# Optimization experiments

Hardware: AMD Instinct MI355X
Metric: run time of the kernel (lower is better)

Reference implementation:

```python
import jax, jax.numpy as jnp
import numpy as np

N_NODES = 100000
N_EDGES = 1600000
IN_CH = 128
TYPE_EMB = 32
OUT_CH = 128
N_REL = 8
N_BASES = 8
N_NTYPES = 8
FEAT = IN_CH + TYPE_EMB  # 160, RGCNConv input dim after concat


def setup_inputs() -> dict:
    key = jax.random.key(0)
    ks = jax.random.split(key, 9)
    x = jax.random.normal(ks[0], (N_NODES, IN_CH), dtype=jnp.float32)
    node_type_ids = jax.random.randint(ks[1], (N_NODES,), 0, N_NTYPES)
    edge_index = jax.random.randint(ks[2], (2, N_EDGES), 0, N_NODES)
    edge_type = jax.random.randint(ks[3], (N_EDGES,), 0, N_REL)
    emb_table = jax.random.normal(ks[4], (N_NTYPES, TYPE_EMB), dtype=jnp.float32)
    bases = jax.random.normal(ks[5], (N_BASES, FEAT, OUT_CH), dtype=jnp.float32) * (1.0 / np.sqrt(FEAT))
    comp = jax.random.normal(ks[6], (N_REL, N_BASES), dtype=jnp.float32) * (1.0 / np.sqrt(N_BASES))
    root_w = jax.random.normal(ks[7], (FEAT, OUT_CH), dtype=jnp.float32) * (1.0 / np.sqrt(FEAT))
    bias = jnp.zeros((OUT_CH,), dtype=jnp.float32)
    return {"x": x, "node_type_ids": node_type_ids, "edge_index": edge_index,
            "edge_type": edge_type, "emb_table": emb_table, "bases": bases,
            "comp": comp, "root_w": root_w, "bias": bias}


def reference(x, node_type_ids, edge_index, edge_type, emb_table, bases, comp, root_w, bias):
    N = x.shape[0]
    # node-type embedding lookup + concat
    h = jnp.concatenate([x, emb_table[node_type_ids]], axis=1)  # [N, FEAT]
    # basis decomposition: per-relation weights [R, FEAT, OUT]
    weight = jnp.einsum('rb,bio->rio', comp, bases)
    src, dst = edge_index[0], edge_index[1]
    h_src = h[src]  # [E, FEAT] -- dominant gather
    # root/self transform + bias
    out = h @ root_w + bias
    # PyG RGCNConv default aggr='mean': per-relation mean over incoming edges, summed across relations
    for r in range(weight.shape[0]):
        m = (edge_type == r).astype(h.dtype)  # [E]
        s = jax.ops.segment_sum(h_src * m[:, None], dst, num_segments=N)  # [N, FEAT]
        c = jax.ops.segment_sum(m, dst, num_segments=N)                    # [N]
        mean_r = s / jnp.maximum(c, 1.0)[:, None]
        out = out + mean_r @ weight[r]
    # dropout is identity in eval mode
    return jax.nn.relu(out)
```

## Files before the change

### kernel.cpp

```cpp
#include <hip/hip_runtime.h>

#define NN 100000
#define NE 1600000
#define INC 128
#define TE 32
#define OC 128
#define NR 8
#define NBASES 8
#define FT 160
#define KP 168
#define KW 160
#define TN 32
#define NBKT 3125
#define NCH 128
#define EPB 12500
#define CAP 896

typedef float f32x4 __attribute__((ext_vector_type(4)));
typedef float f32x2 __attribute__((ext_vector_type(2)));
typedef __bf16 bf16x8 __attribute__((ext_vector_type(8)));

__device__ __forceinline__ unsigned f2bf1(float f) {
    unsigned u = __float_as_uint(f);
    return (u + 0x7fffu + ((u >> 16) & 1u)) >> 16;
}

__device__ __forceinline__ float bflo(unsigned u) { return __uint_as_float(u << 16); }
__device__ __forceinline__ float bfhi(unsigned u) { return __uint_as_float(u & 0xFFFF0000u); }

__device__ __forceinline__ unsigned cvtpk(float a, float b) {
    unsigned r;
    asm("v_cvt_pk_bf16_f32 %0, %1, %2" : "=v"(r) : "v"(a), "v"(b));
    return r;
}

__device__ __forceinline__ int bscan_excl(int v, int* tmp) {
    int tid = threadIdx.x;
    tmp[tid] = v; __syncthreads();
#pragma unroll
    for (int d = 1; d < 256; d <<= 1) {
        int t = (tid >= d) ? tmp[tid - d] : 0;
        __syncthreads();
        tmp[tid] += t;
        __syncthreads();
    }
    return tmp[tid] - v;
}

__global__ __launch_bounds__(256) void k_prep(
    const float* __restrict__ x, const int* __restrict__ nt,
    const float* __restrict__ emb, const float* __restrict__ comp,
    const float* __restrict__ bases, const float* __restrict__ rootw,
    const int* __restrict__ ei,
    unsigned short* __restrict__ h, unsigned short* __restrict__ Wt,
    int* __restrict__ ghist) {
    __shared__ int hist[NBKT];
    int tid = threadIdx.x;
    int b = blockIdx.x;
    if (b < NCH) {
        for (int j = tid; j < NBKT; j += 256) hist[j] = 0;
        __syncthreads();
        int e0 = b * EPB;
#pragma unroll
        for (int k = 0; k < 49; k++) {
            int i = k * 256 + tid;
            if (i < EPB) atomicAdd(&hist[ei[NE + e0 + i] >> 5], 1);
        }
        __syncthreads();
        int* g = ghist + (size_t)b * NBKT;
        for (int j = tid; j < NBKT; j += 256) g[j] = hist[j];
        return;
    }
    int idx = (b - NCH) * 256 + tid;
    if (idx < 9 * 128 * KW) {
        int ridx = idx / (128 * KW);
        int rem  = idx % (128 * KW);
        int o = rem / KW;
        int k = rem % KW;
        float v;
        if (ridx < NR) {
            v = 0.f;
#pragma unroll
            for (int bb = 0; bb < NBASES; bb++)
                v += comp[ridx * NBASES + bb] * bases[(bb * FT + k) * OC + o];
        } else {
            v = rootw[k * OC + o];
        }
        Wt[idx] = (unsigned short)f2bf1(v);
    }
    if (idx < NN * 20) {
        int n = idx / 20, c = idx % 20;
        f32x4 v0, v1;
        if (c < 16) {
            const float* p = x + (size_t)n * INC + c * 8;
            v0 = *(const f32x4*)p; v1 = *(const f32x4*)(p + 4);
        } else {
            int tt = nt[n];
            const float* p = emb + tt * TE + (c - 16) * 8;
            v0 = *(const f32x4*)p; v1 = *(const f32x4*)(p + 4);
        }
        uint4 o;
        o.x = f2bf1(v0.x) | (f2bf1(v0.y) << 16);
        o.y = f2bf1(v0.z) | (f2bf1(v0.w) << 16);
        o.z = f2bf1(v1.x) | (f2bf1(v1.y) << 16);
        o.w = f2bf1(v1.z) | (f2bf1(v1.w) << 16);
        *(uint4*)(h + (size_t)n * FT + c * 8) = o;
    }
}

__global__ void k_total(const int* __restrict__ ghist, int* __restrict__ total) {
    int j = blockIdx.x * 256 + threadIdx.x;
    if (j >= NBKT) return;
    int s = 0;
#pragma unroll 8
    for (int b = 0; b < NCH; b++) s += ghist[(size_t)b * NBKT + j];
    total[j] = s;
}

__global__ void k_scanTot(const int* __restrict__ total, int* __restrict__ bstart) {
    __shared__ int tmp[256];
    int tid = threadIdx.x, s = 0, i0 = tid * 13;
#pragma unroll
    for (int i = 0; i < 13; i++) { int j = i0 + i; if (j < NBKT) s += total[j]; }
    int run = bscan_excl(s, tmp);
#pragma unroll
    for (int i = 0; i < 13; i++) { int j = i0 + i; if (j < NBKT) { bstart[j] = run; run += total[j]; } }
    if (tid == 0) bstart[NBKT] = NE;
}

__global__ void k_offsets(int* __restrict__ ghist, const int* __restrict__ bstart) {
    int j = blockIdx.x * 256 + threadIdx.x;
    if (j >= NBKT) return;
    int run = bstart[j];
#pragma unroll 4
    for (int b = 0; b < NCH; b++) {
        int v = ghist[(size_t)b * NBKT + j];
        ghist[(size_t)b * NBKT + j] = run;
        run += v;
    }
}

__global__ __launch_bounds__(256) void k_scatter(const int* __restrict__ ei, const int* __restrict__ et,
                                                 const int* __restrict__ ghist, unsigned* __restrict__ slots) {
    __shared__ int cur[NBKT];
    int tid = threadIdx.x, b = blockIdx.x;
    for (int j = tid; j < NBKT; j += 256) cur[j] = ghist[(size_t)b * NBKT + j];
    __syncthreads();
    int e0 = b * EPB;
#pragma unroll
    for (int k = 0; k < 49; k++) {
        int i = k * 256 + tid;
        if (i < EPB) {
            int e = e0 + i;
            int s = ei[e], d = ei[NE + e], r = et[e];
            int pos = atomicAdd(&cur[d >> 5], 1);
            slots[pos] = (unsigned)s | ((unsigned)r << 17) | ((unsigned)(d & 31) << 20);
        }
    }
}

__global__ __launch_bounds__(256, 6) void k_mega(
    const unsigned short* __restrict__ h, const float* __restrict__ bias,
    const unsigned short* __restrict__ Wt, const int* __restrict__ bstart,
    const unsigned* __restrict__ slots, float* __restrict__ out) {
    __shared__ unsigned short featmem[TN * KP];
    __shared__ unsigned sl[CAP];
    __shared__ unsigned pkl[256];

    const int tid = threadIdx.x;
    const int lane = tid & 63;
    const int wave = tid >> 6;
    const int j = blockIdx.x;
    const int n0 = j * TN;

    unsigned* sl_in = reinterpret_cast<unsigned*>(featmem);
    int* hist = reinterpret_cast<int*>(featmem) + CAP;
    int* tmp  = reinterpret_cast<int*>(featmem) + CAP + 256;

    int s0 = bstart[j];
    int m = bstart[j + 1] - s0; if (m > CAP) m = CAP;
    for (int i = tid; i < m; i += 256) sl_in[i] = slots[s0 + i];
    hist[tid] = 0;
    __syncthreads();
    for (int i = tid; i < m; i += 256) {
        unsigned v = sl_in[i];
        atomicAdd(&hist[((v >> 17) & 7u) * 32u + ((v >> 20) & 31u)], 1);
    }
    __syncthreads();
    int v0 = hist[tid];
    int ex = bscan_excl(v0, tmp);
    pkl[tid] = (unsigned)ex | ((unsigned)v0 << 16);
    hist[tid] = ex;
    __syncthreads();
    for (int i = tid; i < m; i += 256) {
        unsigned v = sl_in[i];
        int p = atomicAdd(&hist[((v >> 17) & 7u) * 32u + ((v >> 20) & 31u)], 1);
        sl[p] = v & 0x1FFFFu;
    }
    __syncthreads();

    for (int i = tid; i < TN * 20; i += 256) {
        int nl = i / 20, c = i % 20, n = n0 + nl;
        uint4 v = *reinterpret_cast<const uint4*>(h + (size_t)n * FT + c * 8);
        *reinterpret_cast<uint4*>(&featmem[nl * KP + c * 8]) = v;
    }

    f32x4 acc[4];
#pragma unroll
    for (int t = 0; t < 4; t++) acc[t] = (f32x4){0.f, 0.f, 0.f, 0.f};

    auto mfma_pass = [&](int ridx) {
        const unsigned short* fA = featmem + (lane & 15) * KP + ((lane >> 4) * 8);
        const unsigned short* gB = Wt + (size_t)ridx * 128 * KW
                                   + (wave * 32 + (lane & 15)) * KW + ((lane >> 4) * 8);
#pragma unroll
        for (int kc = 0; kc < 5; kc++) {
            bf16x8 a0 = *reinterpret_cast<const bf16x8*>(fA + 0 * 16 * KP + kc * 32);
            bf16x8 a1 = *reinterpret_cast<const bf16x8*>(fA + 1 * 16 * KP + kc * 32);
#pragma unroll
            for (int ct = 0; ct < 2; ct++) {
                bf16x8 b = *reinterpret_cast<const bf16x8*>(gB + ct * 16 * KW + kc * 32);
                acc[0 * 2 + ct] = __builtin_amdgcn_mfma_f32_16x16x32_bf16(a0, b, acc[0 * 2 + ct], 0, 0, 0);
                acc[1 * 2 + ct] = __builtin_amdgcn_mfma_f32_16x16x32_bf16(a1, b, acc[1 * 2 + ct], 0, 0, 0);
            }
        }
    };

    __syncthreads();
    mfma_pass(8);

    const int g = tid >> 4, l = tid & 15;
    const unsigned* hw = reinterpret_cast<const unsigned*>(h);
    for (int r = 0; r < NR; r++) {
        __syncthreads();
        int b0 = r * 32 + 2 * g;
        unsigned pk1 = pkl[b0 + 1];
        int sbeg = (int)(pkl[b0] & 0xffffu);
        int e1 = (int)(pk1 & 0xffffu);
        int send = e1 + (int)(pk1 >> 16);
        f32x2 sa[5];
#pragma unroll
        for (int i = 0; i < 5; i++) sa[i] = (f32x2){0.f, 0.f};
        float run = 0.f;
        for (int e = sbeg; e < send; e += 4) {
            uint4 wv[4]; unsigned tv[4];
#pragma unroll
            for (int u = 0; u < 4; u++) {
                int eu = e + u; if (eu >= send) eu = send - 1;
                const unsigned* hp = hw + (size_t)sl[eu] * 80;
                wv[u] = *reinterpret_cast<const uint4*>(hp + 4 * l);
                tv[u] = hp[64 + l];
            }
#pragma unroll
            for (int u = 0; u < 4; u++) {
                if (e + u < send) {
                    sa[0] += (f32x2){bflo(wv[u].x), bfhi(wv[u].x)};
                    sa[1] += (f32x2){bflo(wv[u].y), bfhi(wv[u].y)};
                    sa[2] += (f32x2){bflo(wv[u].z), bfhi(wv[u].z)};
                    sa[3] += (f32x2){bflo(wv[u].w), bfhi(wv[u].w)};
                    sa[4] += (f32x2){bflo(tv[u]), bfhi(tv[u])};
                    run += 1.f;
                    int nx = e + u + 1;
                    if (nx == e1 || nx == send) {
                        int q = (e + u >= e1) ? 1 : 0;
                        float inv = __builtin_amdgcn_rcpf(run);
                        f32x2 m0 = sa[0] * inv, m1 = sa[1] * inv, m2 = sa[2] * inv,
                              m3 = sa[3] * inv, m4 = sa[4] * inv;
                        unsigned* fp = reinterpret_cast<unsigned*>(featmem + (2 * g + q) * KP);
                        uint4 o;
                        o.x = cvtpk(m0.x, m0.y);
                        o.y = cvtpk(m1.x, m1.y);
                        o.z = cvtpk(m2.x, m2.y);
                        o.w = cvtpk(m3.x, m3.y);
                        *reinterpret_cast<uint4*>(fp + 4 * l) = o;
                        fp[64 + l] = cvtpk(m4.x, m4.y);
#pragma unroll
                        for (int i = 0; i < 5; i++) sa[i] = (f32x2){0.f, 0.f};
                        run = 0.f;
                    }
                }
            }
        }
#pragma unroll
        for (int q = 0; q < 2; q++) {
            if ((pkl[b0 + q] >> 16) == 0u) {
                unsigned* fp = reinterpret_cast<unsigned*>(featmem + (2 * g + q) * KP);
                *reinterpret_cast<uint4*>(fp + 4 * l) = (uint4){0u, 0u, 0u, 0u};
                fp[64 + l] = 0u;
            }
        }
        __syncthreads();
        mfma_pass(r);
    }

    const int rq = lane >> 4;
#pragma unroll
    for (int ct = 0; ct < 2; ct++) {
        int col = wave * 32 + ct * 16 + (lane & 15);
        float bv = bias[col];
#pragma unroll
        for (int rt = 0; rt < 2; rt++) {
#pragma unroll
            for (int i = 0; i < 4; i++) {
                int n = n0 + rt * 16 + rq * 4 + i;
                float v = acc[rt * 2 + ct][i] + bv;
                out[(size_t)n * OC + col] = v > 0.f ? v : 0.f;
            }
        }
    }
}

extern "C" void kernel_launch(void* const* d_in, const int* in_sizes, int n_in,
                              void* d_out, int out_size, void* d_ws, size_t ws_size,
                              hipStream_t stream) {
    const float* x     = (const float*)d_in[0];
    const int*   ntype = (const int*)d_in[1];
    const int*   ei    = (const int*)d_in[2];
    const int*   et    = (const int*)d_in[3];
    const float* emb   = (const float*)d_in[4];
    const float* bases = (const float*)d_in[5];
    const float* comp  = (const float*)d_in[6];
    const float* rootw = (const float*)d_in[7];
    const float* bias  = (const float*)d_in[8];
    float* out = (float*)d_out;

    char* ws = (char*)d_ws;
    unsigned short* Wt     = (unsigned short*)(ws);
    unsigned short* h      = (unsigned short*)(ws + 368640);
    int*            ghist  = (int*)(ws + 32368640);
    int*            total  = (int*)(ws + 33968640);
    int*            bstart = (int*)(ws + 33981184);
    unsigned*       slots  = (unsigned*)(ws + 33993728);

    k_prep   <<<NCH + 7813, 256, 0, stream>>>(x, ntype, emb, comp, bases, rootw, ei, h, Wt, ghist);
    k_total  <<<13,   256, 0, stream>>>(ghist, total);
    k_scanTot<<<1,    256, 0, stream>>>(total, bstart);
    k_offsets<<<13,   256, 0, stream>>>(ghist, bstart);
    k_scatter<<<NCH,  256, 0, stream>>>(ei, et, ghist, slots);
    k_mega   <<<NBKT, 256, 0, stream>>>(h, bias, Wt, bstart, slots, out);
}
```

Before: 349.6 us.

## Double-buffer aggregation/MFMA in mega kernel and fuse histogram scan kernels

The main kernel now uses two shared-memory feature buffers, so aggregating relation r overlaps with the MFMA pass for relation r-1 (or the root weight) and one barrier per iteration goes away. The preprocessing pipeline folds bucket totals into k_prep through global atomics, then merges the scan and per-chunk offset kernels into one 13-block kernel that each redundantly scans the totals. This removes two launches but adds a memset and doubles the LDS feature buffer, which may lower occupancy of k_mega.

```diff
diff --git a/kernel.cpp b/kernel.cpp
--- a/kernel.cpp
+++ b/kernel.cpp
@@ -53,7 +53,7 @@
     const float* __restrict__ bases, const float* __restrict__ rootw,
     const int* __restrict__ ei,
     unsigned short* __restrict__ h, unsigned short* __restrict__ Wt,
-    int* __restrict__ ghist) {
+    int* __restrict__ ghist, int* __restrict__ total) {
     __shared__ int hist[NBKT];
     int tid = threadIdx.x;
     int b = blockIdx.x;
@@ -68,7 +68,11 @@
         }
         __syncthreads();
         int* g = ghist + (size_t)b * NBKT;
-        for (int j = tid; j < NBKT; j += 256) g[j] = hist[j];
+        for (int j = tid; j < NBKT; j += 256) {
+            int v = hist[j];
+            g[j] = v;
+            if (v) atomicAdd(&total[j], v);
+        }
         return;
     }
     int idx = (b - NCH) * 256 + tid;
@@ -108,35 +112,43 @@
     }
 }
 
-__global__ void k_total(const int* __restrict__ ghist, int* __restrict__ total) {
-    int j = blockIdx.x * 256 + threadIdx.x;
-    if (j >= NBKT) return;
-    int s = 0;
-#pragma unroll 8
-    for (int b = 0; b < NCH; b++) s += ghist[(size_t)b * NBKT + j];
-    total[j] = s;
-}
-
-__global__ void k_scanTot(const int* __restrict__ total, int* __restrict__ bstart) {
+__global__ __launch_bounds__(256) void k_scanoff(const int* __restrict__ total,
+                                                 int* __restrict__ ghist,
+                                                 int* __restrict__ bstart) {
+    __shared__ int tot[NBKT];
     __shared__ int tmp[256];
-    int tid = threadIdx.x, s = 0, i0 = tid * 13;
-#pragma unroll
-    for (int i = 0; i < 13; i++) { int j = i0 + i; if (j < NBKT) s += total[j]; }
+    int tid = threadIdx.x;
+    for (int j = tid; j < NBKT; j += 256) tot[j] = total[j];
+    __syncthreads();
+    int i0 = tid * 13, s = 0;
+    int loc[13];
+#pragma unroll
+    for (int i = 0; i < 13; i++) {
+        int j = i0 + i;
+        loc[i] = (j < NBKT) ? tot[j] : 0;
+        s += loc[i];
+    }
     int run = bscan_excl(s, tmp);
 #pragma unroll
-    for (int i = 0; i < 13; i++) { int j = i0 + i; if (j < NBKT) { bstart[j] = run; run += total[j]; } }
-    if (tid == 0) bstart[NBKT] = NE;
-}
-
-__global__ void k_offsets(int* __restrict__ ghist, const int* __restrict__ bstart) {
-    int j = blockIdx.x * 256 + threadIdx.x;
-    if (j >= NBKT) return;
-    int run = bstart[j];
+    for (int i = 0; i < 13; i++) {
+        int j = i0 + i;
+        if (j < NBKT) tot[j] = run;
+        run += loc[i];
+    }
+    __syncthreads();
+    if (blockIdx.x == 0) {
+        for (int j = tid; j < NBKT; j += 256) bstart[j] = tot[j];
+        if (tid == 0) bstart[NBKT] = NE;
+    }
+    int j = blockIdx.x * 256 + tid;
+    if (j < NBKT) {
+        int run2 = tot[j];
 #pragma unroll 4
-    for (int b = 0; b < NCH; b++) {
-        int v = ghist[(size_t)b * NBKT + j];
-        ghist[(size_t)b * NBKT + j] = run;
-        run += v;
+        for (int b = 0; b < NCH; b++) {
+            int v = ghist[(size_t)b * NBKT + j];
+            ghist[(size_t)b * NBKT + j] = run2;
+            run2 += v;
+        }
     }
 }
 
@@ -163,7 +175,7 @@
     const unsigned short* __restrict__ h, const float* __restrict__ bias,
     const unsigned short* __restrict__ Wt, const int* __restrict__ bstart,
     const unsigned* __restrict__ slots, float* __restrict__ out) {
-    __shared__ unsigned short featmem[TN * KP];
+    __shared__ unsigned short featmem[2][TN * KP];
     __shared__ unsigned sl[CAP];
     __shared__ unsigned pkl[256];
 
@@ -173,9 +185,9 @@
     const int j = blockIdx.x;
     const int n0 = j * TN;
 
-    unsigned* sl_in = reinterpret_cast<unsigned*>(featmem);
-    int* hist = reinterpret_cast<int*>(featmem) + CAP;
-    int* tmp  = reinterpret_cast<int*>(featmem) + CAP + 256;
+    unsigned* sl_in = reinterpret_cast<unsigned*>(&featmem[0][0]);
+    int* hist = reinterpret_cast<int*>(&featmem[0][0]) + CAP;
+    int* tmp  = reinterpret_cast<int*>(&featmem[0][0]) + CAP + 256;
 
     int s0 = bstart[j];
     int m = bstart[j + 1] - s0; if (m > CAP) m = CAP;
@@ -202,15 +214,15 @@
     for (int i = tid; i < TN * 20; i += 256) {
         int nl = i / 20, c = i % 20, n = n0 + nl;
         uint4 v = *reinterpret_cast<const uint4*>(h + (size_t)n * FT + c * 8);
-        *reinterpret_cast<uint4*>(&featmem[nl * KP + c * 8]) = v;
+        *reinterpret_cast<uint4*>(&featmem[0][nl * KP + c * 8]) = v;
     }
 
     f32x4 acc[4];
 #pragma unroll
     for (int t = 0; t < 4; t++) acc[t] = (f32x4){0.f, 0.f, 0.f, 0.f};
 
-    auto mfma_pass = [&](int ridx) {
-        const unsigned short* fA = featmem + (lane & 15) * KP + ((lane >> 4) * 8);
+    auto mfma_pass = [&](int ridx, const unsigned short* fm) {
+        const unsigned short* fA = fm + (lane & 15) * KP + ((lane >> 4) * 8);
         const unsigned short* gB = Wt + (size_t)ridx * 128 * KW
                                    + (wave * 32 + (lane & 15)) * KW + ((lane >> 4) * 8);
 #pragma unroll
@@ -226,16 +238,13 @@
         }
     };
 
-    __syncthreads();
-    mfma_pass(8);
-
     const int g = tid >> 4, l = tid & 15;
     const unsigned* hw = reinterpret_cast<const unsigned*>(h);
-    for (int r = 0; r < NR; r++) {
-        __syncthreads();
+
+    auto agg_pass = [&](int r, unsigned short* fm) {
         int b0 = r * 32 + 2 * g;
-        unsigned pk1 = pkl[b0 + 1];
-        int sbeg = (int)(pkl[b0] & 0xffffu);
+        unsigned pk0 = pkl[b0], pk1 = pkl[b0 + 1];
+        int sbeg = (int)(pk0 & 0xffffu);
         int e1 = (int)(pk1 & 0xffffu);
         int send = e1 + (int)(pk1 >> 16);
         f32x2 sa[5];
@@ -266,7 +275,7 @@
                         float inv = __builtin_amdgcn_rcpf(run);
                         f32x2 m0 = sa[0] * inv, m1 = sa[1] * inv, m2 = sa[2] * inv,
                               m3 = sa[3] * inv, m4 = sa[4] * inv;
-                        unsigned* fp = reinterpret_cast<unsigned*>(featmem + (2 * g + q) * KP);
+                        unsigned* fp = reinterpret_cast<unsigned*>(fm + (2 * g + q) * KP);
                         uint4 o;
                         o.x = cvtpk(m0.x, m0.y);
                         o.y = cvtpk(m1.x, m1.y);
@@ -284,14 +293,22 @@
 #pragma unroll
         for (int q = 0; q < 2; q++) {
             if ((pkl[b0 + q] >> 16) == 0u) {
-                unsigned* fp = reinterpret_cast<unsigned*>(featmem + (2 * g + q) * KP);
+                unsigned* fp = reinterpret_cast<unsigned*>(fm + (2 * g + q) * KP);
                 *reinterpret_cast<uint4*>(fp + 4 * l) = (uint4){0u, 0u, 0u, 0u};
                 fp[64 + l] = 0u;
             }
         }
-        __syncthreads();
-        mfma_pass(r);
-    }
+    };
+
+    __syncthreads();
+    int prev = 8;
+    for (int r = 0; r < NR; r++) {
+        agg_pass(r, &featmem[(r + 1) & 1][0]);
+        mfma_pass(prev, &featmem[r & 1][0]);
+        prev = r;
+        __syncthreads();
+    }
+    mfma_pass(7, &featmem[0][0]);
 
     const int rq = lane >> 4;
 #pragma unroll
@@ -332,10 +349,9 @@
     int*            bstart = (int*)(ws + 33981184);
     unsigned*       slots  = (unsigned*)(ws + 33993728);
 
-    k_prep   <<<NCH + 7813, 256, 0, stream>>>(x, ntype, emb, comp, bases, rootw, ei, h, Wt, ghist);
-    k_total  <<<13,   256, 0, stream>>>(ghist, total);
-    k_scanTot<<<1,    256, 0, stream>>>(total, bstart);
-    k_offsets<<<13,   256, 0, stream>>>(ghist, bstart);
+    hipMemsetAsync(total, 0, (NBKT + 1) * sizeof(int), stream);
+    k_prep   <<<NCH + 7813, 256, 0, stream>>>(x, ntype, emb, comp, bases, rootw, ei, h, Wt, ghist, total);
+    k_scanoff<<<13,   256, 0, stream>>>(total, ghist, bstart);
     k_scatter<<<NCH,  256, 0, stream>>>(ei, et, ghist, slots);
     k_mega   <<<NBKT, 256, 0, stream>>>(h, bias, Wt, bstart, slots, out);
 }
```

Measured after the change: 350.3 us. No clear change (+0.2%).
